# Optimization experiments

Measured on AMD Instinct MI355X. Metric: run time of the kernel, lower is better.

The kernel has to match this reference:

```python
import jax, jax.numpy as jnp
import numpy as np

N_NODES = 50000
N_EDGES = 600000
IN_DIM = 128
HID = 128


def setup_inputs() -> dict:
    key = jax.random.key(0)
    ks = jax.random.split(key, 8)
    x = jax.random.normal(ks[0], (N_NODES, IN_DIM), dtype=jnp.float32)
    edge_index = jax.random.randint(ks[1], (2, N_EDGES), 0, N_NODES, dtype=jnp.int64)
    def lin(k, fan_in, fan_out):
        s = 1.0 / np.sqrt(fan_in)
        kw, kb = jax.random.split(k)
        W = jax.random.uniform(kw, (fan_in, fan_out), jnp.float32, -s, s)
        b = jax.random.uniform(kb, (fan_out,), jnp.float32, -s, s)
        return W, b
    W0, b0 = lin(ks[2], IN_DIM, HID)
    W1, b1 = lin(ks[3], HID, HID)
    W2, b2 = lin(ks[4], HID, HID)
    return {"x": x, "edge_index": edge_index, "W0": W0, "b0": b0,
            "W1": W1, "b1": b1, "W2": W2, "b2": b2}


def reference(x, edge_index, W0, b0, W1, b1, W2, b2):
    n = x.shape[0]
    loops = jnp.arange(n, dtype=edge_index.dtype)
    src = jnp.concatenate([edge_index[0], loops])  # source nodes (+self loops)
    dst = jnp.concatenate([edge_index[1], loops])  # destination nodes
    # symmetric GCN normalization: deg^{-1/2}[src] * deg^{-1/2}[dst]
    deg = jax.ops.segment_sum(jnp.ones(src.shape[0], x.dtype), dst, num_segments=n)
    dinv = jnp.where(deg > 0, jax.lax.rsqrt(deg), 0.0)
    norm = dinv[src] * dinv[dst]  # [E+N]

    def gcn_layer(h, W, b):
        hw = h @ W                              # [N, H]
        msg = hw[src] * norm[:, None]           # gather + scale, [E+N, H]
        agg = jax.ops.segment_sum(msg, dst, num_segments=n)  # scatter-add
        return agg + b

    h = x
    for W, b in ((W0, b0), (W1, b1), (W2, b2)):
        h = jax.nn.relu(gcn_layer(h, W, b))     # dropout is identity in eval
    return h  # JK='last'
```

## Files before the change

### kernel.cpp

```cpp
#include <hip/hip_runtime.h>

#define NN 50000
#define NE 600000
#define DIM 128
#define NB_N 196
#define NB_E 2344
#define TILES 3125
#define ROWW 136
#define NEPAD (NE + 8 * NN + 64)

typedef unsigned short u16;
typedef unsigned int u32;
typedef __attribute__((ext_vector_type(8))) short bf16x8;
typedef __attribute__((ext_vector_type(4))) float f32x4;

__device__ __forceinline__ u16 f2bf(float f) {
    u32 u = __builtin_bit_cast(u32, f);
    u32 r = (u + 0x7FFFu + ((u >> 16) & 1u)) >> 16;
    return (u16)r;
}
__device__ __forceinline__ float bflo(u32 w) { return __builtin_bit_cast(float, w << 16); }
__device__ __forceinline__ float bfhi(u32 w) { return __builtin_bit_cast(float, w & 0xffff0000u); }
__device__ __forceinline__ int pad8(int d) {
    int p = (d + 7) & ~7;
    return p < 8 ? 8 : p;
}


__global__ __launch_bounds__(256) void k_count(const int* __restrict__ ei,
                                               int* __restrict__ deg) {
    __shared__ int s64;
    if (threadIdx.x == 0) {
        int o = 0;
#pragma unroll
        for (int j = 0; j < 16; j++) o |= ei[2 * j + 1];
        s64 = (o == 0);
    }
    __syncthreads();
    int e = blockIdx.x * 256 + threadIdx.x;
    if (e >= NE) return;
    int d = s64 ? ei[2 * (NE + e)] : ei[NE + e];
    atomicAdd(&deg[d], 1);
}

__global__ __launch_bounds__(256) void k_scanA(const int* __restrict__ deg,
                                               int* __restrict__ rp8,
                                               int* __restrict__ bsum) {
    __shared__ int buf[256];
    int t = threadIdx.x, i = blockIdx.x * 256 + t;
    int v = (i < NN) ? pad8(deg[i]) : 0;
    buf[t] = v;
    __syncthreads();
    for (int off = 1; off < 256; off <<= 1) {
        int x = (t >= off) ? buf[t - off] : 0;
        __syncthreads();
        buf[t] += x;
        __syncthreads();
    }
    if (i < NN) rp8[i] = buf[t] - v;
    if (t == 255) bsum[blockIdx.x] = buf[255];
}

__global__ __launch_bounds__(256) void k_scanB(int* __restrict__ bsum) {
    __shared__ int buf[256];
    int t = threadIdx.x;
    int v = (t < NB_N) ? bsum[t] : 0;
    buf[t] = v;
    __syncthreads();
    for (int off = 1; off < 256; off <<= 1) {
        int x = (t >= off) ? buf[t - off] : 0;
        __syncthreads();
        buf[t] += x;
        __syncthreads();
    }
    bsum[t] = buf[t] - v;
}

__global__ __launch_bounds__(256) void k_scanC(const int* __restrict__ deg,
                                               int* __restrict__ rp8,
                                               const int* __restrict__ bsum,
                                               float* __restrict__ dinv) {
    int i = blockIdx.x * 256 + threadIdx.x;
    if (i < NN) {
        rp8[i] += bsum[i >> 8];
        dinv[i] = rsqrtf((float)(deg[i] + 1));
    }
    if (i == 0) rp8[NN] = bsum[255];
}

__global__ __launch_bounds__(256) void k_fill(const int* __restrict__ ei,
                                              const int* __restrict__ rp8,
                                              int* __restrict__ cursor,
                                              const int* __restrict__ deg,
                                              int* __restrict__ recs,
                                              const float* __restrict__ W0,
                                              const float* __restrict__ W1,
                                              const float* __restrict__ W2,
                                              u16* __restrict__ Wt,
                                              u16* __restrict__ hwA,
                                              u16* __restrict__ hwB) {
    __shared__ int s64;
    if (threadIdx.x == 0) {
        int o = 0;
#pragma unroll
        for (int j = 0; j < 16; j++) o |= ei[2 * j + 1];
        s64 = (o == 0);
    }
    __syncthreads();
    int e = blockIdx.x * 256 + threadIdx.x;
    if (e < NE) {
        int is64 = s64;
        int s = is64 ? ei[2 * e] : ei[e];
        int d = is64 ? ei[2 * (NE + e)] : ei[NE + e];
        int pos = rp8[d] + atomicAdd(&cursor[d], 1);
        recs[pos] = s;
    }
    int b = blockIdx.x;
    if (b < 192) {
        int idx = b * 256 + threadIdx.x;
        int l = idx >> 14, rem = idx & 16383;
        int n = rem >> 7, k = rem & 127;
        const float* W = (l == 0) ? W0 : ((l == 1) ? W1 : W2);
        Wt[idx] = f2bf(W[k * 128 + n]);
    } else if (b < 388) {
        int i = (b - 192) * 256 + threadIdx.x;
        if (i < NN) {
            int rp = rp8[i], d = deg[i], p = pad8(d);
            for (int j = d; j < p; j++) recs[rp + j] = NN;
        }
    } else if (b == 388) {
        if (threadIdx.x < 64) {
            ((u32*)(hwA + (size_t)NN * DIM))[threadIdx.x] = 0;
            ((u32*)(hwB + (size_t)NN * DIM))[threadIdx.x] = 0;
        }
    }
}

__global__ __launch_bounds__(256) void k_gemm_f32(const float* __restrict__ x,
                                                  const u16* __restrict__ Wt,
                                                  const float* __restrict__ dinv,
                                                  u16* __restrict__ hwb) {
    int lane = threadIdx.x & 63;
    int tile = blockIdx.x * 4 + (threadIdx.x >> 6);
    if (tile >= TILES) return;
    int r = lane & 15, q = lane >> 4;

    bf16x8 Bf[8][4];
#pragma unroll
    for (int nt = 0; nt < 8; nt++)
#pragma unroll
        for (int kc = 0; kc < 4; kc++)
            Bf[nt][kc] = *(const bf16x8*)(Wt + ((nt * 16 + r) << 7) + kc * 32 + q * 8);

    long rowbase = (long)tile * 16;
    bf16x8 Af[4];
#pragma unroll
    for (int kc = 0; kc < 4; kc++) {
        const float4* p = (const float4*)(x + (rowbase + r) * 128 + kc * 32 + q * 8);
        float4 t0 = p[0], t1 = p[1];
        bf16x8 a;
        a[0] = (short)f2bf(t0.x); a[1] = (short)f2bf(t0.y);
        a[2] = (short)f2bf(t0.z); a[3] = (short)f2bf(t0.w);
        a[4] = (short)f2bf(t1.x); a[5] = (short)f2bf(t1.y);
        a[6] = (short)f2bf(t1.z); a[7] = (short)f2bf(t1.w);
        Af[kc] = a;
    }

    float dv[4];
#pragma unroll
    for (int i = 0; i < 4; i++) dv[i] = dinv[rowbase + q * 4 + i];

#pragma unroll
    for (int nt = 0; nt < 8; nt++) {
        f32x4 acc = {0.f, 0.f, 0.f, 0.f};
#pragma unroll
        for (int kc = 0; kc < 4; kc++)
            acc = __builtin_amdgcn_mfma_f32_16x16x32_bf16(Af[kc], Bf[nt][kc], acc, 0, 0, 0);
#pragma unroll
        for (int i = 0; i < 4; i++)
            hwb[(rowbase + q * 4 + i) * 128 + nt * 16 + r] = f2bf(dv[i] * acc[i]);
    }
}

__device__ __forceinline__ void add8(float* a, uint4 u) {
    a[0] += bflo(u.x); a[1] += bfhi(u.x);
    a[2] += bflo(u.y); a[3] += bfhi(u.y);
    a[4] += bflo(u.z); a[5] += bfhi(u.z);
    a[6] += bflo(u.w); a[7] += bfhi(u.w);
}

__device__ __forceinline__ void agg_pair(const u16* __restrict__ hw,
                                         const int* __restrict__ rp8,
                                         const int* __restrict__ recs,
                                         int va, int vb, int g, int r,
                                         float* A, float* B) {
    uint4 sva = *(const uint4*)(hw + (size_t)va * DIM + r * 8);
    uint4 svb = *(const uint4*)(hw + (size_t)vb * DIM + r * 8);
    float m = (g == 0) ? 1.0f : 0.0f;
    A[0] = m * bflo(sva.x); A[1] = m * bfhi(sva.x);
    A[2] = m * bflo(sva.y); A[3] = m * bfhi(sva.y);
    A[4] = m * bflo(sva.z); A[5] = m * bfhi(sva.z);
    A[6] = m * bflo(sva.w); A[7] = m * bfhi(sva.w);
    B[0] = m * bflo(svb.x); B[1] = m * bfhi(svb.x);
    B[2] = m * bflo(svb.y); B[3] = m * bfhi(svb.y);
    B[4] = m * bflo(svb.z); B[5] = m * bfhi(svb.z);
    B[6] = m * bflo(svb.w); B[7] = m * bfhi(svb.w);

    int ea = rp8[va], enda = rp8[va + 1];
    int eb = rp8[vb], endb = rp8[vb + 1];
    int2 qa = *(const int2*)(recs + ea + 2 * g);
    int2 qb = *(const int2*)(recs + eb + 2 * g);
    while (ea < enda || eb < endb) {
        int sa0 = (ea < enda) ? qa.x : NN;
        int sa1 = (ea < enda) ? qa.y : NN;
        int sb0 = (eb < endb) ? qb.x : NN;
        int sb1 = (eb < endb) ? qb.y : NN;
        uint4 ua0 = *(const uint4*)(hw + (size_t)(u32)sa0 * DIM + r * 8);
        uint4 ua1 = *(const uint4*)(hw + (size_t)(u32)sa1 * DIM + r * 8);
        uint4 ub0 = *(const uint4*)(hw + (size_t)(u32)sb0 * DIM + r * 8);
        uint4 ub1 = *(const uint4*)(hw + (size_t)(u32)sb1 * DIM + r * 8);
        ea += 8; eb += 8;
        int2 qa_n = *(const int2*)(recs + min(ea, enda - 8) + 2 * g);
        int2 qb_n = *(const int2*)(recs + min(eb, endb - 8) + 2 * g);
        add8(A, ua0); add8(A, ua1);
        add8(B, ub0); add8(B, ub1);
        qa = qa_n; qb = qb_n;
    }
}

__device__ __forceinline__ void combine_scale(float dv, const float* bias, int r,
                                              float* acc) {
#pragma unroll
    for (int j = 0; j < 8; j++) {
        acc[j] += __shfl_xor(acc[j], 16, 64);
        acc[j] += __shfl_xor(acc[j], 32, 64);
    }
    float4 b0 = ((const float4*)bias)[2 * r];
    float4 b1 = ((const float4*)bias)[2 * r + 1];
    acc[0] = fmaxf(fmaf(dv, acc[0], b0.x), 0.f);
    acc[1] = fmaxf(fmaf(dv, acc[1], b0.y), 0.f);
    acc[2] = fmaxf(fmaf(dv, acc[2], b0.z), 0.f);
    acc[3] = fmaxf(fmaf(dv, acc[3], b0.w), 0.f);
    acc[4] = fmaxf(fmaf(dv, acc[4], b1.x), 0.f);
    acc[5] = fmaxf(fmaf(dv, acc[5], b1.y), 0.f);
    acc[6] = fmaxf(fmaf(dv, acc[6], b1.z), 0.f);
    acc[7] = fmaxf(fmaf(dv, acc[7], b1.w), 0.f);
}

__global__ __launch_bounds__(256) void k_agg_gemm(const u16* __restrict__ hw_in,
                                                  const int* __restrict__ rp8,
                                                  const int* __restrict__ recs,
                                                  const float* __restrict__ dinv,
                                                  const float* __restrict__ bias,
                                                  const u16* __restrict__ Wt,
                                                  u16* __restrict__ hw_out) {
    __shared__ u16 sm[16 * ROWW];
    int lane = threadIdx.x & 63;
    int w = threadIdx.x >> 6;
    int g = lane >> 4, r = lane & 15;
    int base = blockIdx.x * 16;
#pragma unroll
    for (int p = 0; p < 2; p++) {
        int rowa = w * 4 + 2 * p;
        int va = base + rowa;
        float A[8], B[8];
        agg_pair(hw_in, rp8, recs, va, va + 1, g, r, A, B);
        combine_scale(dinv[va], bias, r, A);
        combine_scale(dinv[va + 1], bias, r, B);
        if (g == 0) {
            uint4 pk;
            pk.x = (u32)f2bf(A[0]) | ((u32)f2bf(A[1]) << 16);
            pk.y = (u32)f2bf(A[2]) | ((u32)f2bf(A[3]) << 16);
            pk.z = (u32)f2bf(A[4]) | ((u32)f2bf(A[5]) << 16);
            pk.w = (u32)f2bf(A[6]) | ((u32)f2bf(A[7]) << 16);
            *(uint4*)(sm + rowa * ROWW + r * 8) = pk;
            pk.x = (u32)f2bf(B[0]) | ((u32)f2bf(B[1]) << 16);
            pk.y = (u32)f2bf(B[2]) | ((u32)f2bf(B[3]) << 16);
            pk.z = (u32)f2bf(B[4]) | ((u32)f2bf(B[5]) << 16);
            pk.w = (u32)f2bf(B[6]) | ((u32)f2bf(B[7]) << 16);
            *(uint4*)(sm + (rowa + 1) * ROWW + r * 8) = pk;
        }
    }
    __syncthreads();
    int q = lane >> 4;
    bf16x8 Af[4];
#pragma unroll
    for (int kc = 0; kc < 4; kc++)
        Af[kc] = *(const bf16x8*)(sm + r * ROWW + kc * 32 + q * 8);
    float dv[4];
#pragma unroll
    for (int i = 0; i < 4; i++) dv[i] = dinv[base + q * 4 + i];
#pragma unroll
    for (int t = 0; t < 2; t++) {
        int nt = w * 2 + t;
        f32x4 acc = {0.f, 0.f, 0.f, 0.f};
#pragma unroll
        for (int kc = 0; kc < 4; kc++) {
            bf16x8 Bf = *(const bf16x8*)(Wt + ((nt * 16 + r) << 7) + kc * 32 + q * 8);
            acc = __builtin_amdgcn_mfma_f32_16x16x32_bf16(Af[kc], Bf, acc, 0, 0, 0);
        }
#pragma unroll
        for (int i = 0; i < 4; i++)
            hw_out[(size_t)(base + q * 4 + i) * DIM + nt * 16 + r] = f2bf(dv[i] * acc[i]);
    }
}

__global__ __launch_bounds__(256) void k_agg_out(const u16* __restrict__ hw_in,
                                                 const int* __restrict__ rp8,
                                                 const int* __restrict__ recs,
                                                 const float* __restrict__ dinv,
                                                 const float* __restrict__ bias,
                                                 float* __restrict__ out) {
    int lane = threadIdx.x & 63;
    int w = threadIdx.x >> 6;
    int g = lane >> 4, r = lane & 15;
    int va = blockIdx.x * 8 + w * 2;
    float A[8], B[8];
    agg_pair(hw_in, rp8, recs, va, va + 1, g, r, A, B);
    combine_scale(dinv[va], bias, r, A);
    combine_scale(dinv[va + 1], bias, r, B);
    if (g == 0) {
        float4* p = (float4*)(out + (size_t)va * DIM + r * 8);
        p[0] = make_float4(A[0], A[1], A[2], A[3]);
        p[1] = make_float4(A[4], A[5], A[6], A[7]);
        p = (float4*)(out + (size_t)(va + 1) * DIM + r * 8);
        p[0] = make_float4(B[0], B[1], B[2], B[3]);
        p[1] = make_float4(B[4], B[5], B[6], B[7]);
    }
}


extern "C" void kernel_launch(void* const* d_in, const int* in_sizes, int n_in,
                              void* d_out, int out_size, void* d_ws, size_t ws_size,
                              hipStream_t stream) {
    const float* x = (const float*)d_in[0];
    const int* ei = (const int*)d_in[1];
    const float* W0 = (const float*)d_in[2];
    const float* b0 = (const float*)d_in[3];
    const float* W1 = (const float*)d_in[4];
    const float* b1 = (const float*)d_in[5];
    const float* W2 = (const float*)d_in[6];
    const float* b2 = (const float*)d_in[7];

    char* ws = (char*)d_ws;
    size_t off = 0;
    auto alloc = [&](size_t bytes) -> void* {
        void* p = ws + off;
        off += (bytes + 511) & ~(size_t)511;
        return p;
    };
    int* deg = (int*)alloc(NN * 4);
    int* cursor = (int*)alloc(NN * 4);
    size_t zbytes = off;
    int* recs = (int*)alloc((size_t)NEPAD * 4);
    float* dinv = (float*)alloc(NN * 4);
    int* rp8 = (int*)alloc((NN + 1) * 4);
    int* bsum = (int*)alloc(256 * 4);
    u16* Wt = (u16*)alloc(3 * 128 * 128 * 2);
    u16* hwA = (u16*)alloc((size_t)(NN + 1) * DIM * 2);
    u16* hwB = (u16*)alloc((size_t)(NN + 1) * DIM * 2);

    hipMemsetAsync(ws, 0, zbytes, stream);
    k_count<<<NB_E, 256, 0, stream>>>(ei, deg);
    k_scanA<<<NB_N, 256, 0, stream>>>(deg, rp8, bsum);
    k_scanB<<<1, 256, 0, stream>>>(bsum);
    k_scanC<<<NB_N, 256, 0, stream>>>(deg, rp8, bsum, dinv);
    k_fill<<<NB_E, 256, 0, stream>>>(ei, rp8, cursor, deg, recs,
                                     W0, W1, W2, Wt, hwA, hwB);
    k_gemm_f32<<<(TILES + 3) / 4, 256, 0, stream>>>(x, Wt, dinv, hwA);
    k_agg_gemm<<<TILES, 256, 0, stream>>>(hwA, rp8, recs, dinv, b0,
                                          Wt + 16384, hwB);
    k_agg_gemm<<<TILES, 256, 0, stream>>>(hwB, rp8, recs, dinv, b1,
                                          Wt + 32768, hwA);
    k_agg_out<<<6250, 256, 0, stream>>>(hwA, rp8, recs, dinv, b2,
                                        (float*)d_out);
}
```

Baseline: 272.9 us.

## Merge all pipeline stages into one persistent cooperative kernel with grid syncs

Result: slower. 841.4 us (+208.3%).

```diff
diff --git a/kernel.cpp b/kernel.cpp
--- a/kernel.cpp
+++ b/kernel.cpp
@@ -1,10 +1,12 @@
 #include <hip/hip_runtime.h>
+#include <hip/hip_cooperative_groups.h>
+
+namespace cg = cooperative_groups;
 
 #define NN 50000
 #define NE 600000
 #define DIM 128
-#define NB_N 196
-#define NB_E 2344
+#define NSCAN 196
 #define TILES 3125
 #define ROWW 136
 #define NEPAD (NE + 8 * NN + 64)
@@ -26,161 +28,26 @@
     return p < 8 ? 8 : p;
 }
 
-
-__global__ __launch_bounds__(256) void k_count(const int* __restrict__ ei,
-                                               int* __restrict__ deg) {
-    __shared__ int s64;
-    if (threadIdx.x == 0) {
-        int o = 0;
-#pragma unroll
-        for (int j = 0; j < 16; j++) o |= ei[2 * j + 1];
-        s64 = (o == 0);
-    }
-    __syncthreads();
-    int e = blockIdx.x * 256 + threadIdx.x;
-    if (e >= NE) return;
-    int d = s64 ? ei[2 * (NE + e)] : ei[NE + e];
-    atomicAdd(&deg[d], 1);
-}
-
-__global__ __launch_bounds__(256) void k_scanA(const int* __restrict__ deg,
-                                               int* __restrict__ rp8,
-                                               int* __restrict__ bsum) {
-    __shared__ int buf[256];
-    int t = threadIdx.x, i = blockIdx.x * 256 + t;
-    int v = (i < NN) ? pad8(deg[i]) : 0;
-    buf[t] = v;
-    __syncthreads();
-    for (int off = 1; off < 256; off <<= 1) {
-        int x = (t >= off) ? buf[t - off] : 0;
-        __syncthreads();
-        buf[t] += x;
-        __syncthreads();
-    }
-    if (i < NN) rp8[i] = buf[t] - v;
-    if (t == 255) bsum[blockIdx.x] = buf[255];
-}
-
-__global__ __launch_bounds__(256) void k_scanB(int* __restrict__ bsum) {
-    __shared__ int buf[256];
-    int t = threadIdx.x;
-    int v = (t < NB_N) ? bsum[t] : 0;
-    buf[t] = v;
-    __syncthreads();
-    for (int off = 1; off < 256; off <<= 1) {
-        int x = (t >= off) ? buf[t - off] : 0;
-        __syncthreads();
-        buf[t] += x;
-        __syncthreads();
-    }
-    bsum[t] = buf[t] - v;
-}
-
-__global__ __launch_bounds__(256) void k_scanC(const int* __restrict__ deg,
-                                               int* __restrict__ rp8,
-                                               const int* __restrict__ bsum,
-                                               float* __restrict__ dinv) {
-    int i = blockIdx.x * 256 + threadIdx.x;
-    if (i < NN) {
-        rp8[i] += bsum[i >> 8];
-        dinv[i] = rsqrtf((float)(deg[i] + 1));
-    }
-    if (i == 0) rp8[NN] = bsum[255];
-}
-
-__global__ __launch_bounds__(256) void k_fill(const int* __restrict__ ei,
-                                              const int* __restrict__ rp8,
-                                              int* __restrict__ cursor,
-                                              const int* __restrict__ deg,
-                                              int* __restrict__ recs,
-                                              const float* __restrict__ W0,
-                                              const float* __restrict__ W1,
-                                              const float* __restrict__ W2,
-                                              u16* __restrict__ Wt,
-                                              u16* __restrict__ hwA,
-                                              u16* __restrict__ hwB) {
-    __shared__ int s64;
-    if (threadIdx.x == 0) {
-        int o = 0;
-#pragma unroll
-        for (int j = 0; j < 16; j++) o |= ei[2 * j + 1];
-        s64 = (o == 0);
-    }
-    __syncthreads();
-    int e = blockIdx.x * 256 + threadIdx.x;
-    if (e < NE) {
-        int is64 = s64;
-        int s = is64 ? ei[2 * e] : ei[e];
-        int d = is64 ? ei[2 * (NE + e)] : ei[NE + e];
-        int pos = rp8[d] + atomicAdd(&cursor[d], 1);
-        recs[pos] = s;
-    }
-    int b = blockIdx.x;
-    if (b < 192) {
-        int idx = b * 256 + threadIdx.x;
-        int l = idx >> 14, rem = idx & 16383;
-        int n = rem >> 7, k = rem & 127;
-        const float* W = (l == 0) ? W0 : ((l == 1) ? W1 : W2);
-        Wt[idx] = f2bf(W[k * 128 + n]);
-    } else if (b < 388) {
-        int i = (b - 192) * 256 + threadIdx.x;
-        if (i < NN) {
-            int rp = rp8[i], d = deg[i], p = pad8(d);
-            for (int j = d; j < p; j++) recs[rp + j] = NN;
-        }
-    } else if (b == 388) {
-        if (threadIdx.x < 64) {
-            ((u32*)(hwA + (size_t)NN * DIM))[threadIdx.x] = 0;
-            ((u32*)(hwB + (size_t)NN * DIM))[threadIdx.x] = 0;
-        }
-    }
-}
-
-__global__ __launch_bounds__(256) void k_gemm_f32(const float* __restrict__ x,
-                                                  const u16* __restrict__ Wt,
-                                                  const float* __restrict__ dinv,
-                                                  u16* __restrict__ hwb) {
-    int lane = threadIdx.x & 63;
-    int tile = blockIdx.x * 4 + (threadIdx.x >> 6);
-    if (tile >= TILES) return;
-    int r = lane & 15, q = lane >> 4;
-
-    bf16x8 Bf[8][4];
-#pragma unroll
-    for (int nt = 0; nt < 8; nt++)
-#pragma unroll
-        for (int kc = 0; kc < 4; kc++)
-            Bf[nt][kc] = *(const bf16x8*)(Wt + ((nt * 16 + r) << 7) + kc * 32 + q * 8);
-
-    long rowbase = (long)tile * 16;
-    bf16x8 Af[4];
-#pragma unroll
-    for (int kc = 0; kc < 4; kc++) {
-        const float4* p = (const float4*)(x + (rowbase + r) * 128 + kc * 32 + q * 8);
-        float4 t0 = p[0], t1 = p[1];
-        bf16x8 a;
-        a[0] = (short)f2bf(t0.x); a[1] = (short)f2bf(t0.y);
-        a[2] = (short)f2bf(t0.z); a[3] = (short)f2bf(t0.w);
-        a[4] = (short)f2bf(t1.x); a[5] = (short)f2bf(t1.y);
-        a[6] = (short)f2bf(t1.z); a[7] = (short)f2bf(t1.w);
-        Af[kc] = a;
-    }
-
-    float dv[4];
-#pragma unroll
-    for (int i = 0; i < 4; i++) dv[i] = dinv[rowbase + q * 4 + i];
-
-#pragma unroll
-    for (int nt = 0; nt < 8; nt++) {
-        f32x4 acc = {0.f, 0.f, 0.f, 0.f};
-#pragma unroll
-        for (int kc = 0; kc < 4; kc++)
-            acc = __builtin_amdgcn_mfma_f32_16x16x32_bf16(Af[kc], Bf[nt][kc], acc, 0, 0, 0);
-#pragma unroll
-        for (int i = 0; i < 4; i++)
-            hwb[(rowbase + q * 4 + i) * 128 + nt * 16 + r] = f2bf(dv[i] * acc[i]);
-    }
-}
+struct Params {
+    const int* ei;
+    int* deg;
+    int* recs;
+    float* dinv;
+    int* rp8;
+    int* bsum;
+    u16* Wt;
+    u16* hwA;
+    u16* hwB;
+    const float* x;
+    const float* W0;
+    const float* W1;
+    const float* W2;
+    const float* b0;
+    const float* b1;
+    const float* b2;
+    float* out;
+};
+
 
 __device__ __forceinline__ void add8(float* a, uint4 u) {
     a[0] += bflo(u.x); a[1] += bfhi(u.x);
@@ -247,18 +114,15 @@
     acc[7] = fmaxf(fmaf(dv, acc[7], b1.w), 0.f);
 }
 
-__global__ __launch_bounds__(256) void k_agg_gemm(const u16* __restrict__ hw_in,
-                                                  const int* __restrict__ rp8,
-                                                  const int* __restrict__ recs,
-                                                  const float* __restrict__ dinv,
-                                                  const float* __restrict__ bias,
-                                                  const u16* __restrict__ Wt,
-                                                  u16* __restrict__ hw_out) {
-    __shared__ u16 sm[16 * ROWW];
-    int lane = threadIdx.x & 63;
-    int w = threadIdx.x >> 6;
+__device__ __forceinline__ void agg_gemm_block(int bb, const u16* hw_in,
+                                               const int* rp8, const int* recs,
+                                               const float* dinv,
+                                               const float* bias, const u16* Wt,
+                                               u16* hw_out, u16* sm, int tid) {
+    int lane = tid & 63;
+    int w = tid >> 6;
     int g = lane >> 4, r = lane & 15;
-    int base = blockIdx.x * 16;
+    int base = bb * 16;
 #pragma unroll
     for (int p = 0; p < 2; p++) {
         int rowa = w * 4 + 2 * p;
@@ -305,16 +169,15 @@
     }
 }
 
-__global__ __launch_bounds__(256) void k_agg_out(const u16* __restrict__ hw_in,
-                                                 const int* __restrict__ rp8,
-                                                 const int* __restrict__ recs,
-                                                 const float* __restrict__ dinv,
-                                                 const float* __restrict__ bias,
-                                                 float* __restrict__ out) {
-    int lane = threadIdx.x & 63;
-    int w = threadIdx.x >> 6;
+__device__ __forceinline__ void agg_out_block(int bb, const u16* hw_in,
+                                              const int* rp8, const int* recs,
+                                              const float* dinv,
+                                              const float* bias, float* out,
+                                              int tid) {
+    int lane = tid & 63;
+    int w = tid >> 6;
     int g = lane >> 4, r = lane & 15;
-    int va = blockIdx.x * 8 + w * 2;
+    int va = bb * 8 + w * 2;
     float A[8], B[8];
     agg_pair(hw_in, rp8, recs, va, va + 1, g, r, A, B);
     combine_scale(dinv[va], bias, r, A);
@@ -329,19 +192,161 @@
     }
 }
 
+__device__ __forceinline__ void gemm_f32_tile(int tile, const float* x,
+                                              const u16* Wt, const float* dinv,
+                                              u16* hwb, int lane) {
+    int r = lane & 15, q = lane >> 4;
+    long rowbase = (long)tile * 16;
+    bf16x8 Af[4];
+#pragma unroll
+    for (int kc = 0; kc < 4; kc++) {
+        const float4* p = (const float4*)(x + (rowbase + r) * 128 + kc * 32 + q * 8);
+        float4 t0 = p[0], t1 = p[1];
+        bf16x8 a;
+        a[0] = (short)f2bf(t0.x); a[1] = (short)f2bf(t0.y);
+        a[2] = (short)f2bf(t0.z); a[3] = (short)f2bf(t0.w);
+        a[4] = (short)f2bf(t1.x); a[5] = (short)f2bf(t1.y);
+        a[6] = (short)f2bf(t1.z); a[7] = (short)f2bf(t1.w);
+        Af[kc] = a;
+    }
+    float dv[4];
+#pragma unroll
+    for (int i = 0; i < 4; i++) dv[i] = dinv[rowbase + q * 4 + i];
+#pragma unroll
+    for (int nt = 0; nt < 8; nt++) {
+        f32x4 acc = {0.f, 0.f, 0.f, 0.f};
+#pragma unroll
+        for (int kc = 0; kc < 4; kc++) {
+            bf16x8 Bf = *(const bf16x8*)(Wt + ((nt * 16 + r) << 7) + kc * 32 + q * 8);
+            acc = __builtin_amdgcn_mfma_f32_16x16x32_bf16(Af[kc], Bf, acc, 0, 0, 0);
+        }
+#pragma unroll
+        for (int i = 0; i < 4; i++)
+            hwb[(rowbase + q * 4 + i) * 128 + nt * 16 + r] = f2bf(dv[i] * acc[i]);
+    }
+}
+
+
+__global__ __launch_bounds__(256, 4) void k_all(Params p) {
+    cg::grid_group grid = cg::this_grid();
+    __shared__ u16 sm[16 * ROWW];
+    __shared__ int buf[256];
+    __shared__ int s64s;
+
+    int b = blockIdx.x, t = threadIdx.x, gn = gridDim.x;
+    int gid = b * 256 + t;
+    int stride = gn * 256;
+
+    if (t == 0) {
+        int o = 0;
+#pragma unroll
+        for (int j = 0; j < 16; j++) o |= p.ei[2 * j + 1];
+        s64s = (o == 0);
+    }
+    __syncthreads();
+    int is64 = s64s;
+
+    for (int i = gid; i < 2 * NN; i += stride) p.deg[i] = 0;
+    grid.sync();
+
+    for (int e = gid; e < NE; e += stride) {
+        int d = is64 ? p.ei[2 * (NE + e)] : p.ei[NE + e];
+        atomicAdd(&p.deg[d], 1);
+    }
+    grid.sync();
+
+    for (int blk = b; blk < NSCAN; blk += gn) {
+        int i = blk * 256 + t;
+        int v = (i < NN) ? pad8(p.deg[i]) : 0;
+        buf[t] = v;
+        __syncthreads();
+        for (int off = 1; off < 256; off <<= 1) {
+            int x = (t >= off) ? buf[t - off] : 0;
+            __syncthreads();
+            buf[t] += x;
+            __syncthreads();
+        }
+        if (i < NN) p.rp8[i] = buf[t] - v;
+        if (t == 255) p.bsum[blk] = buf[255];
+        __syncthreads();
+    }
+    grid.sync();
+
+    if (b == 0) {
+        int v = (t < NSCAN) ? p.bsum[t] : 0;
+        buf[t] = v;
+        __syncthreads();
+        for (int off = 1; off < 256; off <<= 1) {
+            int x = (t >= off) ? buf[t - off] : 0;
+            __syncthreads();
+            buf[t] += x;
+            __syncthreads();
+        }
+        p.bsum[t] = buf[t] - v;
+    }
+    grid.sync();
+
+    for (int i = gid; i < NN; i += stride) {
+        p.rp8[i] += p.bsum[i >> 8];
+        p.dinv[i] = rsqrtf((float)(p.deg[i] + 1));
+    }
+    if (gid == 0) p.rp8[NN] = p.bsum[255];
+    grid.sync();
+
+    {
+        int* cursor = p.deg + NN;
+        for (int e = gid; e < NE; e += stride) {
+            int s = is64 ? p.ei[2 * e] : p.ei[e];
+            int d = is64 ? p.ei[2 * (NE + e)] : p.ei[NE + e];
+            int pos = p.rp8[d] + atomicAdd(&cursor[d], 1);
+            p.recs[pos] = s;
+        }
+        for (int idx = gid; idx < 3 * 16384; idx += stride) {
+            int l = idx >> 14, rem = idx & 16383;
+            int n = rem >> 7, k = rem & 127;
+            const float* W = (l == 0) ? p.W0 : ((l == 1) ? p.W1 : p.W2);
+            p.Wt[idx] = f2bf(W[k * 128 + n]);
+        }
+        for (int i = gid; i < NN; i += stride) {
+            int rp = p.rp8[i], d = p.deg[i], pd = pad8(d);
+            for (int j = d; j < pd; j++) p.recs[rp + j] = NN;
+        }
+        if (gid < 64) {
+            ((u32*)(p.hwA + (size_t)NN * DIM))[gid] = 0;
+            ((u32*)(p.hwB + (size_t)NN * DIM))[gid] = 0;
+        }
+    }
+    grid.sync();
+
+    {
+        int w = t >> 6, lane = t & 63;
+        for (int tile = b * 4 + w; tile < TILES; tile += gn * 4)
+            gemm_f32_tile(tile, p.x, p.Wt, p.dinv, p.hwA, lane);
+    }
+    grid.sync();
+
+    for (int bb = b; bb < TILES; bb += gn) {
+        agg_gemm_block(bb, p.hwA, p.rp8, p.recs, p.dinv, p.b0,
+                       p.Wt + 16384, p.hwB, sm, t);
+        __syncthreads();
+    }
+    grid.sync();
+
+    for (int bb = b; bb < TILES; bb += gn) {
+        agg_gemm_block(bb, p.hwB, p.rp8, p.recs, p.dinv, p.b1,
+                       p.Wt + 32768, p.hwA, sm, t);
+        __syncthreads();
+    }
+    grid.sync();
+
+    for (int bb = b; bb < 6250; bb += gn)
+        agg_out_block(bb, p.hwA, p.rp8, p.recs, p.dinv, p.b2, p.out, t);
+}
+
 
 extern "C" void kernel_launch(void* const* d_in, const int* in_sizes, int n_in,
                               void* d_out, int out_size, void* d_ws, size_t ws_size,
                               hipStream_t stream) {
-    const float* x = (const float*)d_in[0];
-    const int* ei = (const int*)d_in[1];
-    const float* W0 = (const float*)d_in[2];
-    const float* b0 = (const float*)d_in[3];
-    const float* W1 = (const float*)d_in[4];
-    const float* b1 = (const float*)d_in[5];
-    const float* W2 = (const float*)d_in[6];
-    const float* b2 = (const float*)d_in[7];
-
     char* ws = (char*)d_ws;
     size_t off = 0;
     auto alloc = [&](size_t bytes) -> void* {
@@ -349,29 +354,32 @@
         off += (bytes + 511) & ~(size_t)511;
         return p;
     };
-    int* deg = (int*)alloc(NN * 4);
-    int* cursor = (int*)alloc(NN * 4);
-    size_t zbytes = off;
-    int* recs = (int*)alloc((size_t)NEPAD * 4);
-    float* dinv = (float*)alloc(NN * 4);
-    int* rp8 = (int*)alloc((NN + 1) * 4);
-    int* bsum = (int*)alloc(256 * 4);
-    u16* Wt = (u16*)alloc(3 * 128 * 128 * 2);
-    u16* hwA = (u16*)alloc((size_t)(NN + 1) * DIM * 2);
-    u16* hwB = (u16*)alloc((size_t)(NN + 1) * DIM * 2);
-
-    hipMemsetAsync(ws, 0, zbytes, stream);
-    k_count<<<NB_E, 256, 0, stream>>>(ei, deg);
-    k_scanA<<<NB_N, 256, 0, stream>>>(deg, rp8, bsum);
-    k_scanB<<<1, 256, 0, stream>>>(bsum);
-    k_scanC<<<NB_N, 256, 0, stream>>>(deg, rp8, bsum, dinv);
-    k_fill<<<NB_E, 256, 0, stream>>>(ei, rp8, cursor, deg, recs,
-                                     W0, W1, W2, Wt, hwA, hwB);
-    k_gemm_f32<<<(TILES + 3) / 4, 256, 0, stream>>>(x, Wt, dinv, hwA);
-    k_agg_gemm<<<TILES, 256, 0, stream>>>(hwA, rp8, recs, dinv, b0,
-                                          Wt + 16384, hwB);
-    k_agg_gemm<<<TILES, 256, 0, stream>>>(hwB, rp8, recs, dinv, b1,
-                                          Wt + 32768, hwA);
-    k_agg_out<<<6250, 256, 0, stream>>>(hwA, rp8, recs, dinv, b2,
-                                        (float*)d_out);
-}
+    Params p;
+    p.ei = (const int*)d_in[1];
+    p.x = (const float*)d_in[0];
+    p.W0 = (const float*)d_in[2];
+    p.b0 = (const float*)d_in[3];
+    p.W1 = (const float*)d_in[4];
+    p.b1 = (const float*)d_in[5];
+    p.W2 = (const float*)d_in[6];
+    p.b2 = (const float*)d_in[7];
+    p.deg = (int*)alloc(2 * NN * 4);
+    p.recs = (int*)alloc((size_t)NEPAD * 4);
+    p.dinv = (float*)alloc(NN * 4);
+    p.rp8 = (int*)alloc((NN + 1) * 4);
+    p.bsum = (int*)alloc(256 * 4);
+    p.Wt = (u16*)alloc(3 * 128 * 128 * 2);
+    p.hwA = (u16*)alloc((size_t)(NN + 1) * DIM * 2);
+    p.hwB = (u16*)alloc((size_t)(NN + 1) * DIM * 2);
+    p.out = (float*)d_out;
+
+    int nb = 0;
+    hipOccupancyMaxActiveBlocksPerMultiprocessor(&nb, (const void*)k_all, 256, 0);
+    if (nb < 1) nb = 1;
+    long g = (long)nb * 256;
+    if (g > 1024) g = 1024;
+    if (g < 256) g = 256;
+    dim3 grid((unsigned)g), block(256);
+    void* args[] = {&p};
+    hipLaunchCooperativeKernel((void*)k_all, grid, block, args, 0, stream);
+}
```

## Stage neighbor rows into LDS via direct global-to-LDS DMA for aggregation

Applied to the files above, without the earlier changes.

After: 358.5 us. +31.4%, slower.

```diff
diff --git a/kernel.cpp b/kernel.cpp
--- a/kernel.cpp
+++ b/kernel.cpp
@@ -7,6 +7,7 @@
 #define NB_E 2344
 #define TILES 3125
 #define ROWW 136
+#define WEDGE 128
 #define NEPAD (NE + 8 * NN + 64)
 
 typedef unsigned short u16;
@@ -24,6 +25,12 @@
 __device__ __forceinline__ int pad8(int d) {
     int p = (d + 7) & ~7;
     return p < 8 ? 8 : p;
+}
+
+__device__ __forceinline__ void dma16(const u16* g, u16* l) {
+    __builtin_amdgcn_global_load_lds(
+        (const __attribute__((address_space(1))) void*)g,
+        (__attribute__((address_space(3))) void*)l, 16, 0, 0);
 }
 
 
@@ -182,150 +189,129 @@
     }
 }
 
-__device__ __forceinline__ void add8(float* a, uint4 u) {
-    a[0] += bflo(u.x); a[1] += bfhi(u.x);
-    a[2] += bflo(u.y); a[3] += bfhi(u.y);
-    a[4] += bflo(u.z); a[5] += bfhi(u.z);
-    a[6] += bflo(u.w); a[7] += bfhi(u.w);
-}
-
-__device__ __forceinline__ void agg_pair(const u16* __restrict__ hw,
-                                         const int* __restrict__ rp8,
-                                         const int* __restrict__ recs,
-                                         int va, int vb, int g, int r,
-                                         float* A, float* B) {
-    uint4 sva = *(const uint4*)(hw + (size_t)va * DIM + r * 8);
-    uint4 svb = *(const uint4*)(hw + (size_t)vb * DIM + r * 8);
-    float m = (g == 0) ? 1.0f : 0.0f;
-    A[0] = m * bflo(sva.x); A[1] = m * bfhi(sva.x);
-    A[2] = m * bflo(sva.y); A[3] = m * bfhi(sva.y);
-    A[4] = m * bflo(sva.z); A[5] = m * bfhi(sva.z);
-    A[6] = m * bflo(sva.w); A[7] = m * bfhi(sva.w);
-    B[0] = m * bflo(svb.x); B[1] = m * bfhi(svb.x);
-    B[2] = m * bflo(svb.y); B[3] = m * bfhi(svb.y);
-    B[4] = m * bflo(svb.z); B[5] = m * bfhi(svb.z);
-    B[6] = m * bflo(svb.w); B[7] = m * bfhi(svb.w);
-
-    int ea = rp8[va], enda = rp8[va + 1];
-    int eb = rp8[vb], endb = rp8[vb + 1];
-    int2 qa = *(const int2*)(recs + ea + 2 * g);
-    int2 qb = *(const int2*)(recs + eb + 2 * g);
-    while (ea < enda || eb < endb) {
-        int sa0 = (ea < enda) ? qa.x : NN;
-        int sa1 = (ea < enda) ? qa.y : NN;
-        int sb0 = (eb < endb) ? qb.x : NN;
-        int sb1 = (eb < endb) ? qb.y : NN;
-        uint4 ua0 = *(const uint4*)(hw + (size_t)(u32)sa0 * DIM + r * 8);
-        uint4 ua1 = *(const uint4*)(hw + (size_t)(u32)sa1 * DIM + r * 8);
-        uint4 ub0 = *(const uint4*)(hw + (size_t)(u32)sb0 * DIM + r * 8);
-        uint4 ub1 = *(const uint4*)(hw + (size_t)(u32)sb1 * DIM + r * 8);
-        ea += 8; eb += 8;
-        int2 qa_n = *(const int2*)(recs + min(ea, enda - 8) + 2 * g);
-        int2 qb_n = *(const int2*)(recs + min(eb, endb - 8) + 2 * g);
-        add8(A, ua0); add8(A, ua1);
-        add8(B, ub0); add8(B, ub1);
-        qa = qa_n; qb = qb_n;
-    }
-}
-
-__device__ __forceinline__ void combine_scale(float dv, const float* bias, int r,
-                                              float* acc) {
-#pragma unroll
-    for (int j = 0; j < 8; j++) {
-        acc[j] += __shfl_xor(acc[j], 16, 64);
-        acc[j] += __shfl_xor(acc[j], 32, 64);
-    }
-    float4 b0 = ((const float4*)bias)[2 * r];
-    float4 b1 = ((const float4*)bias)[2 * r + 1];
-    acc[0] = fmaxf(fmaf(dv, acc[0], b0.x), 0.f);
-    acc[1] = fmaxf(fmaf(dv, acc[1], b0.y), 0.f);
-    acc[2] = fmaxf(fmaf(dv, acc[2], b0.z), 0.f);
-    acc[3] = fmaxf(fmaf(dv, acc[3], b0.w), 0.f);
-    acc[4] = fmaxf(fmaf(dv, acc[4], b1.x), 0.f);
-    acc[5] = fmaxf(fmaf(dv, acc[5], b1.y), 0.f);
-    acc[6] = fmaxf(fmaf(dv, acc[6], b1.z), 0.f);
-    acc[7] = fmaxf(fmaf(dv, acc[7], b1.w), 0.f);
-}
-
-__global__ __launch_bounds__(256) void k_agg_gemm(const u16* __restrict__ hw_in,
-                                                  const int* __restrict__ rp8,
-                                                  const int* __restrict__ recs,
-                                                  const float* __restrict__ dinv,
-                                                  const float* __restrict__ bias,
-                                                  const u16* __restrict__ Wt,
-                                                  u16* __restrict__ hw_out) {
-    __shared__ u16 sm[16 * ROWW];
-    int lane = threadIdx.x & 63;
-    int w = threadIdx.x >> 6;
-    int g = lane >> 4, r = lane & 15;
+__device__ __forceinline__ void agg_tile_dma(const u16* __restrict__ hw_in,
+                                             const int* __restrict__ rp8,
+                                             const int* __restrict__ recs,
+                                             u16* smrows, int base, int w,
+                                             int lane, float acc[4][2]) {
+    int rb[5];
+    {
+        int4 nr = *(const int4*)(rp8 + base + w * 4);
+        rb[0] = nr.x; rb[1] = nr.y; rb[2] = nr.z; rb[3] = nr.w;
+        rb[4] = rp8[base + w * 4 + 4];
+    }
+    int ts = rp8[base], te = rp8[base + 16];
+
+#pragma unroll
+    for (int n = 0; n < 4; n++) {
+        int v = base + w * 4 + n;
+        u32 sv = *(const u32*)(hw_in + (size_t)v * DIM + lane * 2);
+        acc[n][0] = bflo(sv);
+        acc[n][1] = bfhi(sv);
+    }
+
+    int c16 = lane >> 4;
+    int ch = lane & 15;
+    int nw = (te - ts + WEDGE - 1) / WEDGE;
+    for (int wi = 0; wi < nw; wi++) {
+        int win = ts + wi * WEDGE;
+#pragma unroll
+        for (int k = 0; k < 8; k++) {
+            int idx = win + w * 32 + k * 4 + c16;
+            int rec = (idx < te) ? recs[idx] : NN;
+            const u16* g = hw_in + (size_t)(u32)rec * DIM + ch * 8;
+            u16* l = smrows + (w * 32 + k * 4) * DIM;
+            dma16(g, l);
+        }
+        __syncthreads();
+#pragma unroll
+        for (int n = 0; n < 4; n++) {
+            int e0 = max(rb[n], win);
+            int e1 = min(rb[n + 1], win + WEDGE);
+            for (int e = e0; e < e1; e++) {
+                u32 u = *(const u32*)(smrows + (e - win) * DIM + lane * 2);
+                acc[n][0] += bflo(u);
+                acc[n][1] += bfhi(u);
+            }
+        }
+        __syncthreads();
+    }
+}
+
+__global__ __launch_bounds__(256, 4) void k_aggg(const u16* __restrict__ hw_in,
+                                                 const int* __restrict__ rp8,
+                                                 const int* __restrict__ recs,
+                                                 const float* __restrict__ dinv,
+                                                 const float* __restrict__ bias,
+                                                 const u16* __restrict__ Wt,
+                                                 u16* __restrict__ hw_out) {
+    __shared__ u16 smrows[WEDGE * DIM];
+    __shared__ u16 smt[16 * ROWW];
+    int t = threadIdx.x;
+    int w = t >> 6, lane = t & 63;
     int base = blockIdx.x * 16;
-#pragma unroll
-    for (int p = 0; p < 2; p++) {
-        int rowa = w * 4 + 2 * p;
-        int va = base + rowa;
-        float A[8], B[8];
-        agg_pair(hw_in, rp8, recs, va, va + 1, g, r, A, B);
-        combine_scale(dinv[va], bias, r, A);
-        combine_scale(dinv[va + 1], bias, r, B);
-        if (g == 0) {
-            uint4 pk;
-            pk.x = (u32)f2bf(A[0]) | ((u32)f2bf(A[1]) << 16);
-            pk.y = (u32)f2bf(A[2]) | ((u32)f2bf(A[3]) << 16);
-            pk.z = (u32)f2bf(A[4]) | ((u32)f2bf(A[5]) << 16);
-            pk.w = (u32)f2bf(A[6]) | ((u32)f2bf(A[7]) << 16);
-            *(uint4*)(sm + rowa * ROWW + r * 8) = pk;
-            pk.x = (u32)f2bf(B[0]) | ((u32)f2bf(B[1]) << 16);
-            pk.y = (u32)f2bf(B[2]) | ((u32)f2bf(B[3]) << 16);
-            pk.z = (u32)f2bf(B[4]) | ((u32)f2bf(B[5]) << 16);
-            pk.w = (u32)f2bf(B[6]) | ((u32)f2bf(B[7]) << 16);
-            *(uint4*)(sm + (rowa + 1) * ROWW + r * 8) = pk;
-        }
-    }
-    __syncthreads();
-    int q = lane >> 4;
+
+    float acc[4][2];
+    agg_tile_dma(hw_in, rp8, recs, smrows, base, w, lane, acc);
+
+    float2 bb = *(const float2*)(bias + lane * 2);
+#pragma unroll
+    for (int n = 0; n < 4; n++) {
+        int v = base + w * 4 + n;
+        float dv = dinv[v];
+        float r0 = fmaxf(fmaf(dv, acc[n][0], bb.x), 0.f);
+        float r1 = fmaxf(fmaf(dv, acc[n][1], bb.y), 0.f);
+        u32 pk = (u32)f2bf(r0) | ((u32)f2bf(r1) << 16);
+        *(u32*)(smt + (w * 4 + n) * ROWW + lane * 2) = pk;
+    }
+    __syncthreads();
+
+    int r = lane & 15, q = lane >> 4;
     bf16x8 Af[4];
 #pragma unroll
     for (int kc = 0; kc < 4; kc++)
-        Af[kc] = *(const bf16x8*)(sm + r * ROWW + kc * 32 + q * 8);
+        Af[kc] = *(const bf16x8*)(smt + r * ROWW + kc * 32 + q * 8);
     float dv[4];
 #pragma unroll
     for (int i = 0; i < 4; i++) dv[i] = dinv[base + q * 4 + i];
 #pragma unroll
-    for (int t = 0; t < 2; t++) {
-        int nt = w * 2 + t;
-        f32x4 acc = {0.f, 0.f, 0.f, 0.f};
+    for (int tt = 0; tt < 2; tt++) {
+        int nt = w * 2 + tt;
+        f32x4 acc2 = {0.f, 0.f, 0.f, 0.f};
 #pragma unroll
         for (int kc = 0; kc < 4; kc++) {
             bf16x8 Bf = *(const bf16x8*)(Wt + ((nt * 16 + r) << 7) + kc * 32 + q * 8);
-            acc = __builtin_amdgcn_mfma_f32_16x16x32_bf16(Af[kc], Bf, acc, 0, 0, 0);
+            acc2 = __builtin_amdgcn_mfma_f32_16x16x32_bf16(Af[kc], Bf, acc2, 0, 0, 0);
         }
 #pragma unroll
         for (int i = 0; i < 4; i++)
-            hw_out[(size_t)(base + q * 4 + i) * DIM + nt * 16 + r] = f2bf(dv[i] * acc[i]);
-    }
-}
-
-__global__ __launch_bounds__(256) void k_agg_out(const u16* __restrict__ hw_in,
+            hw_out[(size_t)(base + q * 4 + i) * DIM + nt * 16 + r] =
+                f2bf(dv[i] * acc2[i]);
+    }
+}
+
+__global__ __launch_bounds__(256, 4) void k_aggo(const u16* __restrict__ hw_in,
                                                  const int* __restrict__ rp8,
                                                  const int* __restrict__ recs,
                                                  const float* __restrict__ dinv,
                                                  const float* __restrict__ bias,
                                                  float* __restrict__ out) {
-    int lane = threadIdx.x & 63;
-    int w = threadIdx.x >> 6;
-    int g = lane >> 4, r = lane & 15;
-    int va = blockIdx.x * 8 + w * 2;
-    float A[8], B[8];
-    agg_pair(hw_in, rp8, recs, va, va + 1, g, r, A, B);
-    combine_scale(dinv[va], bias, r, A);
-    combine_scale(dinv[va + 1], bias, r, B);
-    if (g == 0) {
-        float4* p = (float4*)(out + (size_t)va * DIM + r * 8);
-        p[0] = make_float4(A[0], A[1], A[2], A[3]);
-        p[1] = make_float4(A[4], A[5], A[6], A[7]);
-        p = (float4*)(out + (size_t)(va + 1) * DIM + r * 8);
-        p[0] = make_float4(B[0], B[1], B[2], B[3]);
-        p[1] = make_float4(B[4], B[5], B[6], B[7]);
+    __shared__ u16 smrows[WEDGE * DIM];
+    int t = threadIdx.x;
+    int w = t >> 6, lane = t & 63;
+    int base = blockIdx.x * 16;
+
+    float acc[4][2];
+    agg_tile_dma(hw_in, rp8, recs, smrows, base, w, lane, acc);
+
+    float2 bb = *(const float2*)(bias + lane * 2);
+#pragma unroll
+    for (int n = 0; n < 4; n++) {
+        int v = base + w * 4 + n;
+        float dv = dinv[v];
+        float r0 = fmaxf(fmaf(dv, acc[n][0], bb.x), 0.f);
+        float r1 = fmaxf(fmaf(dv, acc[n][1], bb.y), 0.f);
+        *(float2*)(out + (size_t)v * DIM + lane * 2) = make_float2(r0, r1);
     }
 }
 
@@ -368,10 +354,10 @@
     k_fill<<<NB_E, 256, 0, stream>>>(ei, rp8, cursor, deg, recs,
                                      W0, W1, W2, Wt, hwA, hwB);
     k_gemm_f32<<<(TILES + 3) / 4, 256, 0, stream>>>(x, Wt, dinv, hwA);
-    k_agg_gemm<<<TILES, 256, 0, stream>>>(hwA, rp8, recs, dinv, b0,
-                                          Wt + 16384, hwB);
-    k_agg_gemm<<<TILES, 256, 0, stream>>>(hwB, rp8, recs, dinv, b1,
-                                          Wt + 32768, hwA);
-    k_agg_out<<<6250, 256, 0, stream>>>(hwA, rp8, recs, dinv, b2,
-                                        (float*)d_out);
-}
+    k_aggg<<<TILES, 256, 0, stream>>>(hwA, rp8, recs, dinv, b0,
+                                      Wt + 16384, hwB);
+    k_aggg<<<TILES, 256, 0, stream>>>(hwB, rp8, recs, dinv, b1,
+                                      Wt + 32768, hwA);
+    k_aggo<<<TILES, 256, 0, stream>>>(hwA, rp8, recs, dinv, b2,
+                                      (float*)d_out);
+}
```
